# Optimization experiments

Hardware: AMD Instinct MI355X
Metric: run time of the kernel (lower is better)

Reference implementation:

```python
import jax, jax.numpy as jnp
import numpy as np

B, S, HID = 1, 2048, 2048
H = 16
D_NOPE, D_ROPE, D_V = 128, 64, 128
Q_HEAD = D_NOPE + D_ROPE  # 192
QL, KVL = 1536, 512
EPS = 1e-6
SCALE = Q_HEAD ** -0.5


def rms_norm(x, w, eps=EPS):
    return x * jax.lax.rsqrt(jnp.mean(x * x, axis=-1, keepdims=True) + eps) * w


def rotate_half(x):
    h = x.shape[-1] // 2
    return jnp.concatenate([-x[..., h:], x[..., :h]], axis=-1)


def apply_rope(x, cos, sin):
    # DeepSeek de-interleave: view(..., d//2, 2).transpose(-1,-2).reshape == [even, odd]
    x = jnp.concatenate([x[..., 0::2], x[..., 1::2]], axis=-1)
    return x * cos + rotate_half(x) * sin


def setup_inputs() -> dict:
    key = jax.random.key(0)
    ks = jax.random.split(key, 8)
    x = jax.random.normal(ks[0], (B, S, HID), dtype=jnp.float32)
    # causal additive mask
    causal = jnp.tril(jnp.ones((S, S), dtype=bool))
    mask = jnp.where(causal, 0.0, -1e9).astype(jnp.float32)[None, None]
    position_ids = jnp.broadcast_to(jnp.arange(S, dtype=jnp.int32), (B, S))
    # RoPE caches, theta=10000
    inv_freq = 1.0 / (10000.0 ** (np.arange(0, D_ROPE, 2, dtype=np.float32) / D_ROPE))
    freqs = np.outer(np.arange(S, dtype=np.float32), inv_freq)
    emb = np.concatenate([freqs, freqs], axis=-1)
    cos = jnp.asarray(np.cos(emb), dtype=jnp.float32)
    sin = jnp.asarray(np.sin(emb), dtype=jnp.float32)
    w = lambda k, shp: (jax.random.normal(k, shp, dtype=jnp.float32) * 0.02)
    return {
        "x": x, "mask": mask, "position_ids": position_ids, "cos": cos, "sin": sin,
        "q_a_w": w(ks[1], (HID, QL)),
        "q_a_ln": jnp.ones((QL,), jnp.float32),
        "q_b_w": w(ks[2], (QL, H * Q_HEAD)),
        "kv_a_w": w(ks[3], (HID, KVL + D_ROPE)),
        "kv_a_ln": jnp.ones((KVL,), jnp.float32),
        "kv_b_w": w(ks[4], (KVL, H * (D_NOPE + D_V))),
        "o_w": w(ks[5], (H * D_V, HID)),
    }


def reference(x, mask, position_ids, cos, sin, q_a_w, q_a_ln, q_b_w, kv_a_w, kv_a_ln, kv_b_w, o_w):
    b, s, _ = x.shape
    # low-rank Q projection
    q = rms_norm(x @ q_a_w, q_a_ln) @ q_b_w            # [B,S,H*192]
    q = q.reshape(b, s, H, Q_HEAD).transpose(0, 2, 1, 3)  # [B,H,S,192]
    q_nope, q_pe = q[..., :D_NOPE], q[..., D_NOPE:]
    # compressed KV + decoupled rope key (MQA, shared across heads)
    ckv = x @ kv_a_w                                   # [B,S,512+64]
    c_norm = rms_norm(ckv[..., :KVL], kv_a_ln)         # [B,S,512]
    k_pe = ckv[..., KVL:][:, None]                     # [B,1,S,64]
    kv = (c_norm @ kv_b_w).reshape(b, s, H, D_NOPE + D_V).transpose(0, 2, 1, 3)
    k_nope, value = kv[..., :D_NOPE], kv[..., D_NOPE:]  # [B,H,S,128] each
    # rope
    cos_p = cos[position_ids][:, None]                 # [B,1,S,64]
    sin_p = sin[position_ids][:, None]
    q_pe = apply_rope(q_pe, cos_p, sin_p)
    k_pe = apply_rope(k_pe, cos_p, sin_p)
    query = jnp.concatenate([q_nope, q_pe], axis=-1)   # [B,H,S,192]
    key = jnp.concatenate([k_nope, jnp.broadcast_to(k_pe, (b, H, s, D_ROPE))], axis=-1)
    scores = jnp.einsum("bhsd,bhtd->bhst", query, key) * SCALE + mask
    attn = jax.nn.softmax(scores, axis=-1)
    out = jnp.einsum("bhst,bhtd->bhsd", attn, value)   # [B,H,S,128]
    out = out.transpose(0, 2, 1, 3).reshape(b, s, H * D_V) @ o_w
    kv_cache = jnp.concatenate([c_norm, k_pe[:, 0]], axis=-1)  # [B,S,576] latent cache
    return out, kv_cache
```

## Files before the change

kernel.cpp:

```cpp
#include <hip/hip_runtime.h>

typedef unsigned short u16;
typedef __bf16 bf16x8 __attribute__((ext_vector_type(8)));
typedef short s16x4 __attribute__((ext_vector_type(4)));
typedef short s16x8 __attribute__((ext_vector_type(8)));
typedef float f32x4 __attribute__((ext_vector_type(4)));

#define S_LEN 2048
#define NHEAD 16
#define QHEAD 192
#define EPS 1e-6f
#define ATTN_SCALE 0.07216878364870323f
#define QSCALE_LOG2E 0.10412011228586118f

__device__ __forceinline__ u16 f2bf(float f) {
    unsigned u = __builtin_bit_cast(unsigned, f);
    u = (u + 0x7FFFu + ((u >> 16) & 1u)) >> 16;
    return (u16)u;
}
__device__ __forceinline__ float bf2f(u16 h) {
    unsigned u = ((unsigned)h) << 16;
    return __builtin_bit_cast(float, u);
}

__device__ __forceinline__ void gl_lds16(const u16* g, u16* l) {
    __builtin_amdgcn_global_load_lds(
        (const __attribute__((address_space(1))) unsigned int*)g,
        (__attribute__((address_space(3))) unsigned int*)l,
        16, 0, 0);
}

#if defined(__has_builtin) && __has_builtin(__builtin_amdgcn_mfma_f32_16x16x16bf16_1k)
__device__ __forceinline__ f32x4 mfma16(s16x4 a, s16x4 b, f32x4 c) {
    return __builtin_amdgcn_mfma_f32_16x16x16bf16_1k(a, b, c, 0, 0, 0);
}
#else
__device__ __forceinline__ f32x4 mfma16(s16x4 a, s16x4 b, f32x4 c) {
    asm volatile("v_mfma_f32_16x16x16_bf16 %0, %1, %2, %0"
                 : "+v"(c) : "v"(a), "v"(b));
    return c;
}
#endif

template <int CF32>
__device__ __forceinline__ void gemm_core(
    u16* __restrict__ smem,
    const u16* __restrict__ A, const u16* __restrict__ B, void* __restrict__ Cv,
    int K, int lda, int ldb, int ldc, int tm, int tn)
{
    const int tid = threadIdx.x;
    const int w = tid >> 6, lane = tid & 63;
    const int q = lane >> 4, r = lane & 15;

    const int lr = lane & 15;
    const int lc = (lane >> 4) * 8;
    const long ld = (w < 4) ? (long)lda : (long)ldb;
    const u16* g0 = ((w < 4)
        ? A + (long)(tm * 128 + w * 32 + lr) * lda
        : B + (long)(tn * 128 + (w - 4) * 32 + lr) * ldb) + lc;
    const u16* g1 = g0 + 16 * ld;
    const int s0 = w * 1024;
    const int s1 = s0 + 512;

    f32x4 acc[4][2] = {};
    const int wm = w >> 2;
    const int wn = w & 3;
    const int n = K >> 5;

    gl_lds16(g0, smem + s0);
    gl_lds16(g1, smem + s1);
    gl_lds16(g0 + 32, smem + 8192 + s0);
    gl_lds16(g1 + 32, smem + 8192 + s1);
    asm volatile("s_waitcnt vmcnt(2)" ::: "memory");
    __builtin_amdgcn_sched_barrier(0);
    __builtin_amdgcn_s_barrier();
    __builtin_amdgcn_sched_barrier(0);

    int bc = 0;
    for (int t = 0; t < n; ++t) {
        u16* const cur = smem + bc * 8192;
        if (t + 2 < n) {
            int bn = bc + 2; if (bn >= 3) bn -= 3;
            u16* const nxt = smem + bn * 8192;
            const long k2 = (long)(t + 2) << 5;
            gl_lds16(g0 + k2, nxt + s0);
            gl_lds16(g1 + k2, nxt + s1);
        }
        bf16x8 af[4], bv[2];
        #pragma unroll
        for (int mt = 0; mt < 4; ++mt)
            af[mt] = *(const bf16x8*)&cur[(wm * 4 + mt) * 512 + lane * 8];
        #pragma unroll
        for (int nt = 0; nt < 2; ++nt)
            bv[nt] = *(const bf16x8*)&cur[4096 + (wn * 2 + nt) * 512 + lane * 8];
        #pragma unroll
        for (int mt = 0; mt < 4; ++mt)
            #pragma unroll
            for (int nt = 0; nt < 2; ++nt)
                acc[mt][nt] = __builtin_amdgcn_mfma_f32_16x16x32_bf16(
                    af[mt], bv[nt], acc[mt][nt], 0, 0, 0);
        if (t + 1 < n) {
            if (t + 2 < n) asm volatile("s_waitcnt vmcnt(2)" ::: "memory");
            else           asm volatile("s_waitcnt vmcnt(0)" ::: "memory");
            __builtin_amdgcn_sched_barrier(0);
            __builtin_amdgcn_s_barrier();
            __builtin_amdgcn_sched_barrier(0);
        }
        if (++bc == 3) bc = 0;
    }

    const int row0 = tm * 128 + wm * 64 + q * 4;
    const int col0 = tn * 128 + wn * 32 + r;
    if (CF32) {
        float* C = (float*)Cv;
        #pragma unroll
        for (int mt = 0; mt < 4; ++mt)
            #pragma unroll
            for (int i = 0; i < 4; ++i) {
                long rb = (long)(row0 + mt * 16 + i) * ldc + col0;
                #pragma unroll
                for (int nt = 0; nt < 2; ++nt)
                    C[rb + nt * 16] = acc[mt][nt][i];
            }
    } else {
        u16* C = (u16*)Cv;
        #pragma unroll
        for (int mt = 0; mt < 4; ++mt)
            #pragma unroll
            for (int i = 0; i < 4; ++i) {
                long rb = (long)(row0 + mt * 16 + i) * ldc + col0;
                #pragma unroll
                for (int nt = 0; nt < 2; ++nt)
                    C[rb + nt * 16] = f2bf(acc[mt][nt][i]);
            }
    }
}

template <int CF32>
__global__ __launch_bounds__(512, 4)
void gemm_bt(const u16* __restrict__ A, const u16* __restrict__ B,
             void* __restrict__ Cv, int K, int lda, int ldb, int ldc)
{
    __shared__ __align__(16) u16 smem[3 * 8192];
    gemm_core<CF32>(smem, A, B, Cv, K, lda, ldb, ldc, blockIdx.y, blockIdx.x);
}

__global__ __launch_bounds__(512, 4)
void gemm_bt_dual(const u16* __restrict__ A0, const u16* __restrict__ B0,
                  void* __restrict__ C0, int K0, int lda0, int ldb0, int ldc0, int nx0,
                  const u16* __restrict__ A1, const u16* __restrict__ B1,
                  void* __restrict__ C1, int K1, int lda1, int ldb1, int ldc1, int nx1)
{
    __shared__ __align__(16) u16 smem[3 * 8192];
    if (blockIdx.z == 0) {
        if ((int)blockIdx.x >= nx0) return;
        gemm_core<0>(smem, A0, B0, C0, K0, lda0, ldb0, ldc0, blockIdx.y, blockIdx.x);
    } else {
        if ((int)blockIdx.x >= nx1) return;
        gemm_core<0>(smem, A1, B1, C1, K1, lda1, ldb1, ldc1, blockIdx.y, blockIdx.x);
    }
}

template<int C0, int C1>
__device__ __forceinline__ void stage_tile(
    const u16* __restrict__ kvb, const u16* __restrict__ kpe,
    const u16* __restrict__ vt,
    u16* __restrict__ Kl, u16* __restrict__ Vl,
    int h, int t, int quad, int r)
{
    #pragma unroll
    for (int c = C0; c < C1; ++c) {
        if (c < 24) {
            const int mtk = c / 6, kc = c % 6;
            const int row = t * 64 + mtk * 16 + r;
            const u16* src = (kc < 4)
                ? kvb + (size_t)row * 4096 + h * 256 + kc * 32 + quad * 8
                : kpe + (size_t)row * 64 + (kc - 4) * 32 + quad * 8;
            gl_lds16(src, &Kl[c * 512]);
        } else {
            const int cv = c - 24, mtd = cv >> 1, sc = cv & 1;
            const u16* src = vt + ((size_t)h * 128 + mtd * 16 + r) * 2048
                             + t * 64 + sc * 32 + quad * 8;
            gl_lds16(src, &Vl[cv * 512]);
        }
    }
}

__device__ __forceinline__ void stage_dispatch(
    const u16* __restrict__ kvb, const u16* __restrict__ kpe,
    const u16* __restrict__ vt,
    u16* __restrict__ Kl, u16* __restrict__ Vl,
    int w, int h, int t, int quad, int r)
{
    if (w == 0)      stage_tile<0, 10>(kvb, kpe, vt, Kl, Vl, h, t, quad, r);
    else if (w == 1) stage_tile<10, 20>(kvb, kpe, vt, Kl, Vl, h, t, quad, r);
    else if (w == 2) stage_tile<20, 30>(kvb, kpe, vt, Kl, Vl, h, t, quad, r);
    else             stage_tile<30, 40>(kvb, kpe, vt, Kl, Vl, h, t, quad, r);
}

__device__ __forceinline__ void kv_tile_step(
    const u16* __restrict__ Kl, const u16* __restrict__ Vl,
    const bf16x8 (&Qf)[6], f32x4 (&Oacc)[8], float& lsum,
    int lane, int quad, int r, int kglob0, int qg, bool maskT)
{
    f32x4 Sacc[4];
    #pragma unroll
    for (int mtk = 0; mtk < 4; ++mtk)
        Sacc[mtk] = (f32x4){0.f, 0.f, 0.f, 0.f};
    #pragma unroll
    for (int kc = 0; kc < 6; ++kc)
        #pragma unroll
        for (int mtk = 0; mtk < 4; ++mtk) {
            bf16x8 Ak = *(const bf16x8*)&Kl[(mtk * 6 + kc) * 512 + lane * 8];
            Sacc[mtk] = __builtin_amdgcn_mfma_f32_16x16x32_bf16(
                Ak, Qf[kc], Sacc[mtk], 0, 0, 0);
        }
    #pragma unroll
    for (int sc = 0; sc < 2; ++sc) {
        s16x4 Pf[2];
        #pragma unroll
        for (int half = 0; half < 2; ++half) {
            const int kb = sc * 2 + half;
            const int kb0 = kglob0 + kb * 16 + quad * 4;
            #pragma unroll
            for (int i = 0; i < 4; ++i) {
                float pv = exp2f(Sacc[kb][i]);
                if (maskT && (kb0 + i > qg)) pv = 0.f;
                lsum += pv;
                Pf[half][i] = (short)f2bf(pv);
            }
        }
        #pragma unroll
        for (int mtd = 0; mtd < 8; ++mtd) {
            s16x8 Av8 = *(const s16x8*)&Vl[(mtd * 2 + sc) * 512 + quad * 128 + r * 8];
            s16x4 lo = __builtin_shufflevector(Av8, Av8, 0, 1, 2, 3);
            s16x4 hi = __builtin_shufflevector(Av8, Av8, 4, 5, 6, 7);
            Oacc[mtd] = mfma16(lo, Pf[0], Oacc[mtd]);
            Oacc[mtd] = mfma16(hi, Pf[1], Oacc[mtd]);
        }
    }
}

__global__ __launch_bounds__(256, 2)
void flash_attn(const u16* __restrict__ query, const u16* __restrict__ kvb,
                const u16* __restrict__ kpe, const u16* __restrict__ vt,
                u16* __restrict__ ao)
{
    const int tid = threadIdx.x;
    const int w = tid >> 6, lane = tid & 63;
    const int quad = lane >> 4, r = lane & 15;

    const int bid = (int)blockIdx.x;
    const int i = bid & 255;
    const int t_ = i >> 4;
    const int h = i & 15;
    const int j = (bid < 256) ? (31 - t_) : t_;

    const int q0 = j * 64;
    const int ntk = j + 1;

    __shared__ __align__(16) u16 smem[40960];

    const int qg = q0 + w * 16 + r;

    bf16x8 Qf[6];
    #pragma unroll
    for (int kc = 0; kc < 6; ++kc)
        Qf[kc] = *(const bf16x8*)(query
            + ((size_t)h * S_LEN + q0 + w * 16 + r) * QHEAD
            + kc * 32 + quad * 8);

    f32x4 Oacc[8];
    #pragma unroll
    for (int mtd = 0; mtd < 8; ++mtd)
        Oacc[mtd] = (f32x4){0.f, 0.f, 0.f, 0.f};
    float lsum = 0.f;

    stage_dispatch(kvb, kpe, vt, smem, smem + 12288, w, h, 0, quad, r);
    __syncthreads();

    for (int t = 0; t < ntk; ++t) {
        u16* const curb = smem + (t & 1) * 20480;
        u16* const nxtb = smem + ((t + 1) & 1) * 20480;
        if (t + 1 < ntk)
            stage_dispatch(kvb, kpe, vt, nxtb, nxtb + 12288, w, h, t + 1, quad, r);
        kv_tile_step(curb, curb + 12288, Qf, Oacc, lsum,
                     lane, quad, r, t * 64, qg, t == ntk - 1);
        __syncthreads();
    }

    float l = lsum;
    l += __shfl_xor(l, 16, 64);
    l += __shfl_xor(l, 32, 64);
    const float inv = 1.0f / l;
    const int qrow = q0 + w * 16 + r;
    #pragma unroll
    for (int mtd = 0; mtd < 8; ++mtd) {
        ushort4 o;
        o.x = f2bf(Oacc[mtd][0] * inv);
        o.y = f2bf(Oacc[mtd][1] * inv);
        o.z = f2bf(Oacc[mtd][2] * inv);
        o.w = f2bf(Oacc[mtd][3] * inv);
        *(ushort4*)(ao + (size_t)qrow * 2048 + h * 128 + mtd * 16 + quad * 4) = o;
    }
}

__global__ __launch_bounds__(256)
void cvt_f32_bf16(const float4* __restrict__ in, ushort4* __restrict__ out, int n4)
{
    int i = blockIdx.x * 256 + threadIdx.x;
    if (i < n4) {
        float4 v = in[i];
        ushort4 o;
        o.x = f2bf(v.x); o.y = f2bf(v.y); o.z = f2bf(v.z); o.w = f2bf(v.w);
        out[i] = o;
    }
}

__global__ __launch_bounds__(256)
void wtrans_k(const float* __restrict__ in, u16* __restrict__ out, int K, int N)
{
    __shared__ float tile[32][33];
    int k0 = blockIdx.x * 32, n0 = blockIdx.y * 32;
    int tx = threadIdx.x, ty = threadIdx.y;
    #pragma unroll
    for (int j = 0; j < 32; j += 8) {
        int n = n0 + tx;
        tile[ty + j][tx] = (n < N) ? in[(long)(k0 + ty + j) * N + n] : 0.0f;
    }
    __syncthreads();
    #pragma unroll
    for (int j = 0; j < 32; j += 8)
        out[(long)(n0 + ty + j) * K + k0 + tx] = f2bf(tile[tx][ty + j]);
}

__global__ __launch_bounds__(256)
void rmsnorm_k(u16* __restrict__ X, const float* __restrict__ w, int D, int ld)
{
    u16* row = X + (long)blockIdx.x * ld;
    const int tid = threadIdx.x;
    __shared__ float red[4];
    float sum = 0.f;
    for (int d = tid; d < D; d += 256) { float v = bf2f(row[d]); sum += v * v; }
    #pragma unroll
    for (int o = 32; o; o >>= 1) sum += __shfl_xor(sum, o, 64);
    if ((tid & 63) == 0) red[tid >> 6] = sum;
    __syncthreads();
    sum = red[0] + red[1] + red[2] + red[3];
    float scale = rsqrtf(sum / (float)D + EPS);
    for (int d = tid; d < D; d += 256)
        row[d] = f2bf(bf2f(row[d]) * scale * w[d]);
}

__global__ __launch_bounds__(256)
void kvcache_k(const u16* __restrict__ qkv, const float* __restrict__ ln,
               const int* __restrict__ pos_ids, const float* __restrict__ cosb,
               const float* __restrict__ sinb, float* __restrict__ kvout,
               u16* __restrict__ cnb, u16* __restrict__ kpe)
{
    const int s = blockIdx.x, tid = threadIdx.x;
    const u16* row = qkv + (long)s * 2176 + 1536;
    __shared__ float red[4];
    float sum = 0.f;
    for (int d = tid; d < 512; d += 256) { float v = bf2f(row[d]); sum += v * v; }
    #pragma unroll
    for (int o = 32; o; o >>= 1) sum += __shfl_xor(sum, o, 64);
    if ((tid & 63) == 0) red[tid >> 6] = sum;
    __syncthreads();
    sum = red[0] + red[1] + red[2] + red[3];
    float scale = rsqrtf(sum / 512.f + EPS);
    for (int d = tid; d < 512; d += 256) {
        float v = bf2f(row[d]) * scale * ln[d];
        kvout[(long)s * 576 + d] = v;
        cnb[(long)s * 512 + d] = f2bf(v);
    }
    if (tid < 32) {
        int p = pos_ids[s];
        float x0 = bf2f(row[512 + 2 * tid]);
        float x1 = bf2f(row[512 + 2 * tid + 1]);
        float c1 = cosb[p * 64 + tid], s1 = sinb[p * 64 + tid];
        float c2 = cosb[p * 64 + 32 + tid], s2 = sinb[p * 64 + 32 + tid];
        float lo = x0 * c1 - x1 * s1;
        float hi = x1 * c2 + x0 * s2;
        kvout[(long)s * 576 + 512 + tid] = lo;
        kvout[(long)s * 576 + 544 + tid] = hi;
        kpe[(long)s * 64 + tid] = f2bf(lo);
        kpe[(long)s * 64 + 32 + tid] = f2bf(hi);
    }
}

__global__ __launch_bounds__(256)
void qrope_k(const u16* __restrict__ qb, const int* __restrict__ pos_ids,
             const float* __restrict__ cosb, const float* __restrict__ sinb,
             u16* __restrict__ query)
{
    const int s = blockIdx.x, tid = threadIdx.x;
    const u16* row = qb + (long)s * 3072;
    {
        int h = tid >> 4, c = tid & 15;
        const u16* src = &row[h * QHEAD + c * 8];
        u16* dst = &query[((long)(h * S_LEN + s)) * QHEAD + c * 8];
        ushort4 a = *(const ushort4*)src;
        ushort4 b = *(const ushort4*)(src + 4);
        ushort4 oa, ob;
        oa.x = f2bf(bf2f(a.x) * QSCALE_LOG2E); oa.y = f2bf(bf2f(a.y) * QSCALE_LOG2E);
        oa.z = f2bf(bf2f(a.z) * QSCALE_LOG2E); oa.w = f2bf(bf2f(a.w) * QSCALE_LOG2E);
        ob.x = f2bf(bf2f(b.x) * QSCALE_LOG2E); ob.y = f2bf(bf2f(b.y) * QSCALE_LOG2E);
        ob.z = f2bf(bf2f(b.z) * QSCALE_LOG2E); ob.w = f2bf(bf2f(b.w) * QSCALE_LOG2E);
        *(ushort4*)dst = oa;
        *(ushort4*)(dst + 4) = ob;
    }
    int p = pos_ids[s];
    for (int idx = tid; idx < 512; idx += 256) {
        int h = idx >> 5, i = idx & 31;
        float x0 = bf2f(row[h * QHEAD + 128 + 2 * i]);
        float x1 = bf2f(row[h * QHEAD + 128 + 2 * i + 1]);
        float c1 = cosb[p * 64 + i], s1 = sinb[p * 64 + i];
        float c2 = cosb[p * 64 + 32 + i], s2 = sinb[p * 64 + 32 + i];
        u16* qr = query + ((long)(h * S_LEN + s)) * QHEAD;
        qr[128 + i] = f2bf((x0 * c1 - x1 * s1) * QSCALE_LOG2E);
        qr[160 + i] = f2bf((x1 * c2 + x0 * s2) * QSCALE_LOG2E);
    }
}

__global__ __launch_bounds__(256)
void vtrans_k(const u16* __restrict__ kv, u16* __restrict__ vt)
{
    __shared__ u16 tile[32][33];
    int s0 = blockIdx.x * 32, d0 = blockIdx.y * 32, h = blockIdx.z;
    int tx = threadIdx.x, ty = threadIdx.y;
    #pragma unroll
    for (int j = 0; j < 32; j += 8)
        tile[ty + j][tx] = kv[(long)(s0 + ty + j) * 4096 + h * 256 + 128 + d0 + tx];
    __syncthreads();
    const int txp = ((tx >> 2) & 3) * 8 + (tx >> 4) * 4 + (tx & 3);
    #pragma unroll
    for (int j = 0; j < 32; j += 8)
        vt[(long)(h * 128 + d0 + ty + j) * S_LEN + s0 + txp] = tile[tx][ty + j];
}

extern "C" void kernel_launch(void* const* d_in, const int* in_sizes, int n_in,
                              void* d_out, int out_size, void* d_ws, size_t ws_size,
                              hipStream_t stream)
{
    const float* x      = (const float*)d_in[0];
    const int*   posid  = (const int*)d_in[2];
    const float* cosb   = (const float*)d_in[3];
    const float* sinb   = (const float*)d_in[4];
    const float* q_a_w  = (const float*)d_in[5];
    const float* q_a_ln = (const float*)d_in[6];
    const float* q_b_w  = (const float*)d_in[7];
    const float* kv_a_w = (const float*)d_in[8];
    const float* kv_a_ln= (const float*)d_in[9];
    const float* kv_b_w = (const float*)d_in[10];
    const float* o_w    = (const float*)d_in[11];

    float* out    = (float*)d_out;
    float* kv_out = out + (size_t)2048 * 2048;

    char* ws = (char*)d_ws;
    size_t off = 0;
    auto alloc = [&](size_t bytes) { char* p = ws + off; off += (bytes + 255) & ~(size_t)255; return p; };
    u16* xb    = (u16*)alloc(2048ULL * 2048 * 2);
    u16* W1    = (u16*)alloc(2176ULL * 2048 * 2);
    u16* qbwt  = (u16*)alloc(3072ULL * 1536 * 2);
    u16* kvbwt = (u16*)alloc(4096ULL * 512 * 2);
    u16* owt   = (u16*)alloc(2048ULL * 2048 * 2);
    u16* qkv_a = (u16*)alloc(2048ULL * 2176 * 2);
    u16* qbuf  = (u16*)alloc(2048ULL * 3072 * 2);
    u16* query = (u16*)alloc(16ULL * 2048 * 192 * 2);
    u16* cnb   = (u16*)alloc(2048ULL * 512 * 2);
    u16* kpe   = (u16*)alloc(2048ULL * 64 * 2);
    u16* kvbuf = (u16*)alloc(2048ULL * 4096 * 2);
    u16* vt    = (u16*)alloc(16ULL * 128 * 2048 * 2);
    u16* ao    = (u16*)alloc(2048ULL * 2048 * 2);
    (void)ws_size; (void)in_sizes; (void)n_in; (void)out_size;

    dim3 blk(256);
    dim3 gblk(512);
    dim3 tblk(32, 8);

    cvt_f32_bf16<<<dim3(4096), blk, 0, stream>>>((const float4*)x, (ushort4*)xb, 2048 * 2048 / 4);
    wtrans_k<<<dim3(64, 48),  tblk, 0, stream>>>(q_a_w,  W1,                    2048, 1536);
    wtrans_k<<<dim3(64, 20),  tblk, 0, stream>>>(kv_a_w, W1 + 1536ULL * 2048,   2048, 576);
    wtrans_k<<<dim3(48, 96),  tblk, 0, stream>>>(q_b_w,  qbwt,  1536, 3072);
    wtrans_k<<<dim3(16, 128), tblk, 0, stream>>>(kv_b_w, kvbwt, 512,  4096);
    wtrans_k<<<dim3(64, 64),  tblk, 0, stream>>>(o_w,    owt,   2048, 2048);

    gemm_bt<0><<<dim3(17, 16), gblk, 0, stream>>>(xb, W1, qkv_a, 2048, 2048, 2048, 2176);
    rmsnorm_k<<<dim3(2048), blk, 0, stream>>>(qkv_a, q_a_ln, 1536, 2176);
    kvcache_k<<<dim3(2048), blk, 0, stream>>>(qkv_a, kv_a_ln, posid, cosb, sinb, kv_out, cnb, kpe);

    gemm_bt_dual<<<dim3(32, 16, 2), gblk, 0, stream>>>(
        qkv_a, qbwt, qbuf, 1536, 2176, 1536, 3072, 24,
        cnb, kvbwt, kvbuf, 512, 512, 512, 4096, 32);
    qrope_k<<<dim3(2048), blk, 0, stream>>>(qbuf, posid, cosb, sinb, query);
    vtrans_k<<<dim3(64, 4, 16), tblk, 0, stream>>>(kvbuf, vt);

    flash_attn<<<dim3(512), dim3(256), 0, stream>>>(query, kvbuf, kpe, vt, ao);

    gemm_bt<1><<<dim3(16, 16), gblk, 0, stream>>>(ao, owt, out, 2048, 2048, 2048, 2048);
}
```

Measured before the change: 397.4 us.

## Fuse prep/norm/post kernels and double per-wave tile work in GEMM and attention

Merges the input cast and five weight transposes into one launch, the two RMSNorm kernels into one, and the q-rope and V-transpose kernels into one, cutting the launch count. The GEMM drops from 8 to 4 waves per block, with each wave computing a 64x64 sub-tile instead of 64x32 and issuing both A and B loads. Flash attention drops from 4 to 2 waves, each handling 32 query rows so every K fragment read from LDS feeds two MFMAs. The larger per-wave tiles raise register pressure and lower occupancy, which could reduce latency hiding.

```diff
diff --git a/kernel.cpp b/kernel.cpp
--- a/kernel.cpp
+++ b/kernel.cpp
@@ -54,24 +54,27 @@
 
     const int lr = lane & 15;
     const int lc = (lane >> 4) * 8;
-    const long ld = (w < 4) ? (long)lda : (long)ldb;
-    const u16* g0 = ((w < 4)
-        ? A + (long)(tm * 128 + w * 32 + lr) * lda
-        : B + (long)(tn * 128 + (w - 4) * 32 + lr) * ldb) + lc;
-    const u16* g1 = g0 + 16 * ld;
-    const int s0 = w * 1024;
-    const int s1 = s0 + 512;
-
-    f32x4 acc[4][2] = {};
-    const int wm = w >> 2;
-    const int wn = w & 3;
+    const u16* ga0 = A + (long)(tm * 128 + w * 32 + lr) * lda + lc;
+    const u16* ga1 = ga0 + 16 * (long)lda;
+    const u16* gb0 = B + (long)(tn * 128 + w * 32 + lr) * ldb + lc;
+    const u16* gb1 = gb0 + 16 * (long)ldb;
+    const int sa0 = w * 1024, sa1 = sa0 + 512;
+    const int sb0 = 4096 + w * 1024, sb1 = sb0 + 512;
+
+    f32x4 acc[4][4] = {};
+    const int wm = w >> 1;
+    const int wn = w & 1;
     const int n = K >> 5;
 
-    gl_lds16(g0, smem + s0);
-    gl_lds16(g1, smem + s1);
-    gl_lds16(g0 + 32, smem + 8192 + s0);
-    gl_lds16(g1 + 32, smem + 8192 + s1);
-    asm volatile("s_waitcnt vmcnt(2)" ::: "memory");
+    gl_lds16(ga0, smem + sa0);
+    gl_lds16(ga1, smem + sa1);
+    gl_lds16(gb0, smem + sb0);
+    gl_lds16(gb1, smem + sb1);
+    gl_lds16(ga0 + 32, smem + 8192 + sa0);
+    gl_lds16(ga1 + 32, smem + 8192 + sa1);
+    gl_lds16(gb0 + 32, smem + 8192 + sb0);
+    gl_lds16(gb1 + 32, smem + 8192 + sb1);
+    asm volatile("s_waitcnt vmcnt(4)" ::: "memory");
     __builtin_amdgcn_sched_barrier(0);
     __builtin_amdgcn_s_barrier();
     __builtin_amdgcn_sched_barrier(0);
@@ -83,24 +86,26 @@
             int bn = bc + 2; if (bn >= 3) bn -= 3;
             u16* const nxt = smem + bn * 8192;
             const long k2 = (long)(t + 2) << 5;
-            gl_lds16(g0 + k2, nxt + s0);
-            gl_lds16(g1 + k2, nxt + s1);
-        }
-        bf16x8 af[4], bv[2];
+            gl_lds16(ga0 + k2, nxt + sa0);
+            gl_lds16(ga1 + k2, nxt + sa1);
+            gl_lds16(gb0 + k2, nxt + sb0);
+            gl_lds16(gb1 + k2, nxt + sb1);
+        }
+        bf16x8 af[4], bv[4];
         #pragma unroll
         for (int mt = 0; mt < 4; ++mt)
             af[mt] = *(const bf16x8*)&cur[(wm * 4 + mt) * 512 + lane * 8];
         #pragma unroll
-        for (int nt = 0; nt < 2; ++nt)
-            bv[nt] = *(const bf16x8*)&cur[4096 + (wn * 2 + nt) * 512 + lane * 8];
+        for (int nt = 0; nt < 4; ++nt)
+            bv[nt] = *(const bf16x8*)&cur[4096 + (wn * 4 + nt) * 512 + lane * 8];
         #pragma unroll
         for (int mt = 0; mt < 4; ++mt)
             #pragma unroll
-            for (int nt = 0; nt < 2; ++nt)
+            for (int nt = 0; nt < 4; ++nt)
                 acc[mt][nt] = __builtin_amdgcn_mfma_f32_16x16x32_bf16(
                     af[mt], bv[nt], acc[mt][nt], 0, 0, 0);
         if (t + 1 < n) {
-            if (t + 2 < n) asm volatile("s_waitcnt vmcnt(2)" ::: "memory");
+            if (t + 2 < n) asm volatile("s_waitcnt vmcnt(4)" ::: "memory");
             else           asm volatile("s_waitcnt vmcnt(0)" ::: "memory");
             __builtin_amdgcn_sched_barrier(0);
             __builtin_amdgcn_s_barrier();
@@ -110,7 +115,7 @@
     }
 
     const int row0 = tm * 128 + wm * 64 + q * 4;
-    const int col0 = tn * 128 + wn * 32 + r;
+    const int col0 = tn * 128 + wn * 64 + r;
     if (CF32) {
         float* C = (float*)Cv;
         #pragma unroll
@@ -119,7 +124,7 @@
             for (int i = 0; i < 4; ++i) {
                 long rb = (long)(row0 + mt * 16 + i) * ldc + col0;
                 #pragma unroll
-                for (int nt = 0; nt < 2; ++nt)
+                for (int nt = 0; nt < 4; ++nt)
                     C[rb + nt * 16] = acc[mt][nt][i];
             }
     } else {
@@ -130,14 +135,14 @@
             for (int i = 0; i < 4; ++i) {
                 long rb = (long)(row0 + mt * 16 + i) * ldc + col0;
                 #pragma unroll
-                for (int nt = 0; nt < 2; ++nt)
+                for (int nt = 0; nt < 4; ++nt)
                     C[rb + nt * 16] = f2bf(acc[mt][nt][i]);
             }
     }
 }
 
 template <int CF32>
-__global__ __launch_bounds__(512, 4)
+__global__ __launch_bounds__(256, 2)
 void gemm_bt(const u16* __restrict__ A, const u16* __restrict__ B,
              void* __restrict__ Cv, int K, int lda, int ldb, int ldc)
 {
@@ -145,7 +150,7 @@
     gemm_core<CF32>(smem, A, B, Cv, K, lda, ldb, ldc, blockIdx.y, blockIdx.x);
 }
 
-__global__ __launch_bounds__(512, 4)
+__global__ __launch_bounds__(256, 2)
 void gemm_bt_dual(const u16* __restrict__ A0, const u16* __restrict__ B0,
                   void* __restrict__ C0, int K0, int lda0, int ldb0, int ldc0, int nx0,
                   const u16* __restrict__ A1, const u16* __restrict__ B1,
@@ -192,42 +197,48 @@
     u16* __restrict__ Kl, u16* __restrict__ Vl,
     int w, int h, int t, int quad, int r)
 {
-    if (w == 0)      stage_tile<0, 10>(kvb, kpe, vt, Kl, Vl, h, t, quad, r);
-    else if (w == 1) stage_tile<10, 20>(kvb, kpe, vt, Kl, Vl, h, t, quad, r);
-    else if (w == 2) stage_tile<20, 30>(kvb, kpe, vt, Kl, Vl, h, t, quad, r);
-    else             stage_tile<30, 40>(kvb, kpe, vt, Kl, Vl, h, t, quad, r);
+    if (w == 0) stage_tile<0, 20>(kvb, kpe, vt, Kl, Vl, h, t, quad, r);
+    else        stage_tile<20, 40>(kvb, kpe, vt, Kl, Vl, h, t, quad, r);
 }
 
 __device__ __forceinline__ void kv_tile_step(
     const u16* __restrict__ Kl, const u16* __restrict__ Vl,
-    const bf16x8 (&Qf)[6], f32x4 (&Oacc)[8], float& lsum,
-    int lane, int quad, int r, int kglob0, int qg, bool maskT)
-{
-    f32x4 Sacc[4];
-    #pragma unroll
-    for (int mtk = 0; mtk < 4; ++mtk)
-        Sacc[mtk] = (f32x4){0.f, 0.f, 0.f, 0.f};
+    const bf16x8 (&Qf)[2][6], f32x4 (&Oacc)[8][2], float (&lsum)[2],
+    int lane, int quad, int r, int kglob0, int qg0, int qg1, bool maskT)
+{
+    f32x4 Sacc[4][2];
+    #pragma unroll
+    for (int mtk = 0; mtk < 4; ++mtk) {
+        Sacc[mtk][0] = (f32x4){0.f, 0.f, 0.f, 0.f};
+        Sacc[mtk][1] = (f32x4){0.f, 0.f, 0.f, 0.f};
+    }
     #pragma unroll
     for (int kc = 0; kc < 6; ++kc)
         #pragma unroll
         for (int mtk = 0; mtk < 4; ++mtk) {
             bf16x8 Ak = *(const bf16x8*)&Kl[(mtk * 6 + kc) * 512 + lane * 8];
-            Sacc[mtk] = __builtin_amdgcn_mfma_f32_16x16x32_bf16(
-                Ak, Qf[kc], Sacc[mtk], 0, 0, 0);
+            Sacc[mtk][0] = __builtin_amdgcn_mfma_f32_16x16x32_bf16(
+                Ak, Qf[0][kc], Sacc[mtk][0], 0, 0, 0);
+            Sacc[mtk][1] = __builtin_amdgcn_mfma_f32_16x16x32_bf16(
+                Ak, Qf[1][kc], Sacc[mtk][1], 0, 0, 0);
         }
     #pragma unroll
     for (int sc = 0; sc < 2; ++sc) {
-        s16x4 Pf[2];
-        #pragma unroll
-        for (int half = 0; half < 2; ++half) {
-            const int kb = sc * 2 + half;
-            const int kb0 = kglob0 + kb * 16 + quad * 4;
+        s16x4 Pf[2][2];
+        #pragma unroll
+        for (int nn = 0; nn < 2; ++nn) {
+            const int qg = nn ? qg1 : qg0;
             #pragma unroll
-            for (int i = 0; i < 4; ++i) {
-                float pv = exp2f(Sacc[kb][i]);
-                if (maskT && (kb0 + i > qg)) pv = 0.f;
-                lsum += pv;
-                Pf[half][i] = (short)f2bf(pv);
+            for (int half = 0; half < 2; ++half) {
+                const int kb = sc * 2 + half;
+                const int kb0 = kglob0 + kb * 16 + quad * 4;
+                #pragma unroll
+                for (int i = 0; i < 4; ++i) {
+                    float pv = exp2f(Sacc[kb][nn][i]);
+                    if (maskT && (kb0 + i > qg)) pv = 0.f;
+                    lsum[nn] += pv;
+                    Pf[nn][half][i] = (short)f2bf(pv);
+                }
             }
         }
         #pragma unroll
@@ -235,13 +246,15 @@
             s16x8 Av8 = *(const s16x8*)&Vl[(mtd * 2 + sc) * 512 + quad * 128 + r * 8];
             s16x4 lo = __builtin_shufflevector(Av8, Av8, 0, 1, 2, 3);
             s16x4 hi = __builtin_shufflevector(Av8, Av8, 4, 5, 6, 7);
-            Oacc[mtd] = mfma16(lo, Pf[0], Oacc[mtd]);
-            Oacc[mtd] = mfma16(hi, Pf[1], Oacc[mtd]);
-        }
-    }
-}
-
-__global__ __launch_bounds__(256, 2)
+            Oacc[mtd][0] = mfma16(lo, Pf[0][0], Oacc[mtd][0]);
+            Oacc[mtd][0] = mfma16(hi, Pf[0][1], Oacc[mtd][0]);
+            Oacc[mtd][1] = mfma16(lo, Pf[1][0], Oacc[mtd][1]);
+            Oacc[mtd][1] = mfma16(hi, Pf[1][1], Oacc[mtd][1]);
+        }
+    }
+}
+
+__global__ __launch_bounds__(128, 1)
 void flash_attn(const u16* __restrict__ query, const u16* __restrict__ kvb,
                 const u16* __restrict__ kpe, const u16* __restrict__ vt,
                 u16* __restrict__ ao)
@@ -261,20 +274,25 @@
 
     __shared__ __align__(16) u16 smem[40960];
 
-    const int qg = q0 + w * 16 + r;
-
-    bf16x8 Qf[6];
-    #pragma unroll
-    for (int kc = 0; kc < 6; ++kc)
-        Qf[kc] = *(const bf16x8*)(query
-            + ((size_t)h * S_LEN + q0 + w * 16 + r) * QHEAD
-            + kc * 32 + quad * 8);
-
-    f32x4 Oacc[8];
-    #pragma unroll
-    for (int mtd = 0; mtd < 8; ++mtd)
-        Oacc[mtd] = (f32x4){0.f, 0.f, 0.f, 0.f};
-    float lsum = 0.f;
+    const int qg0 = q0 + w * 32 + r;
+    const int qg1 = qg0 + 16;
+
+    bf16x8 Qf[2][6];
+    #pragma unroll
+    for (int nn = 0; nn < 2; ++nn)
+        #pragma unroll
+        for (int kc = 0; kc < 6; ++kc)
+            Qf[nn][kc] = *(const bf16x8*)(query
+                + ((size_t)h * S_LEN + q0 + w * 32 + nn * 16 + r) * QHEAD
+                + kc * 32 + quad * 8);
+
+    f32x4 Oacc[8][2];
+    #pragma unroll
+    for (int mtd = 0; mtd < 8; ++mtd) {
+        Oacc[mtd][0] = (f32x4){0.f, 0.f, 0.f, 0.f};
+        Oacc[mtd][1] = (f32x4){0.f, 0.f, 0.f, 0.f};
+    }
+    float lsum[2] = {0.f, 0.f};
 
     stage_dispatch(kvb, kpe, vt, smem, smem + 12288, w, h, 0, quad, r);
     __syncthreads();
@@ -285,99 +303,110 @@
         if (t + 1 < ntk)
             stage_dispatch(kvb, kpe, vt, nxtb, nxtb + 12288, w, h, t + 1, quad, r);
         kv_tile_step(curb, curb + 12288, Qf, Oacc, lsum,
-                     lane, quad, r, t * 64, qg, t == ntk - 1);
+                     lane, quad, r, t * 64, qg0, qg1, t == ntk - 1);
         __syncthreads();
     }
 
-    float l = lsum;
-    l += __shfl_xor(l, 16, 64);
-    l += __shfl_xor(l, 32, 64);
-    const float inv = 1.0f / l;
-    const int qrow = q0 + w * 16 + r;
-    #pragma unroll
-    for (int mtd = 0; mtd < 8; ++mtd) {
-        ushort4 o;
-        o.x = f2bf(Oacc[mtd][0] * inv);
-        o.y = f2bf(Oacc[mtd][1] * inv);
-        o.z = f2bf(Oacc[mtd][2] * inv);
-        o.w = f2bf(Oacc[mtd][3] * inv);
-        *(ushort4*)(ao + (size_t)qrow * 2048 + h * 128 + mtd * 16 + quad * 4) = o;
-    }
+    #pragma unroll
+    for (int nn = 0; nn < 2; ++nn) {
+        float l = lsum[nn];
+        l += __shfl_xor(l, 16, 64);
+        l += __shfl_xor(l, 32, 64);
+        const float inv = 1.0f / l;
+        const int qrow = q0 + w * 32 + nn * 16 + r;
+        #pragma unroll
+        for (int mtd = 0; mtd < 8; ++mtd) {
+            ushort4 o;
+            o.x = f2bf(Oacc[mtd][nn][0] * inv);
+            o.y = f2bf(Oacc[mtd][nn][1] * inv);
+            o.z = f2bf(Oacc[mtd][nn][2] * inv);
+            o.w = f2bf(Oacc[mtd][nn][3] * inv);
+            *(ushort4*)(ao + (size_t)qrow * 2048 + h * 128 + mtd * 16 + quad * 4) = o;
+        }
+    }
+}
+
+__device__ __forceinline__ void wtrans_body(
+    float (*tile)[33], const float* __restrict__ in, u16* __restrict__ out,
+    int K, int N, int bx, int by, int tid)
+{
+    const int tx = tid & 31, ty = tid >> 5;
+    const int k0 = bx * 32, n0 = by * 32;
+    #pragma unroll
+    for (int jj = 0; jj < 32; jj += 8) {
+        int nn = n0 + tx;
+        tile[ty + jj][tx] = (nn < N) ? in[(long)(k0 + ty + jj) * N + nn] : 0.0f;
+    }
+    __syncthreads();
+    #pragma unroll
+    for (int jj = 0; jj < 32; jj += 8)
+        out[(long)(n0 + ty + jj) * K + k0 + tx] = f2bf(tile[tx][ty + jj]);
 }
 
 __global__ __launch_bounds__(256)
-void cvt_f32_bf16(const float4* __restrict__ in, ushort4* __restrict__ out, int n4)
-{
-    int i = blockIdx.x * 256 + threadIdx.x;
-    if (i < n4) {
-        float4 v = in[i];
+void prep_k(const float4* __restrict__ x4, ushort4* __restrict__ xb4,
+            const float* __restrict__ q_a_w, const float* __restrict__ kv_a_w,
+            const float* __restrict__ q_b_w, const float* __restrict__ kv_b_w,
+            const float* __restrict__ o_w,
+            u16* __restrict__ W1, u16* __restrict__ qbwt,
+            u16* __restrict__ kvbwt, u16* __restrict__ owt)
+{
+    __shared__ float tile[32][33];
+    const int tid = threadIdx.x;
+    int b = (int)blockIdx.x;
+    if (b < 4096) {
+        int i = b * 256 + tid;
+        float4 v = x4[i];
         ushort4 o;
         o.x = f2bf(v.x); o.y = f2bf(v.y); o.z = f2bf(v.z); o.w = f2bf(v.w);
-        out[i] = o;
-    }
+        xb4[i] = o;
+        return;
+    }
+    b -= 4096;
+    if (b < 3072)       wtrans_body(tile, q_a_w,  W1,                  2048, 1536, b % 64, b / 64, tid);
+    else if ((b -= 3072) < 1280) wtrans_body(tile, kv_a_w, W1 + 1536ULL * 2048, 2048, 576,  b % 64, b / 64, tid);
+    else if ((b -= 1280) < 4608) wtrans_body(tile, q_b_w,  qbwt,       1536, 3072, b % 48, b / 48, tid);
+    else if ((b -= 4608) < 2048) wtrans_body(tile, kv_b_w, kvbwt,      512,  4096, b % 16, b / 16, tid);
+    else { b -= 2048;            wtrans_body(tile, o_w,    owt,        2048, 2048, b % 64, b / 64, tid); }
 }
 
 __global__ __launch_bounds__(256)
-void wtrans_k(const float* __restrict__ in, u16* __restrict__ out, int K, int N)
-{
-    __shared__ float tile[32][33];
-    int k0 = blockIdx.x * 32, n0 = blockIdx.y * 32;
-    int tx = threadIdx.x, ty = threadIdx.y;
-    #pragma unroll
-    for (int j = 0; j < 32; j += 8) {
-        int n = n0 + tx;
-        tile[ty + j][tx] = (n < N) ? in[(long)(k0 + ty + j) * N + n] : 0.0f;
-    }
-    __syncthreads();
-    #pragma unroll
-    for (int j = 0; j < 32; j += 8)
-        out[(long)(n0 + ty + j) * K + k0 + tx] = f2bf(tile[tx][ty + j]);
-}
-
-__global__ __launch_bounds__(256)
-void rmsnorm_k(u16* __restrict__ X, const float* __restrict__ w, int D, int ld)
-{
-    u16* row = X + (long)blockIdx.x * ld;
-    const int tid = threadIdx.x;
-    __shared__ float red[4];
+void norm_k(u16* __restrict__ qkv, const float* __restrict__ q_ln,
+            const float* __restrict__ kv_ln, const int* __restrict__ pos_ids,
+            const float* __restrict__ cosb, const float* __restrict__ sinb,
+            float* __restrict__ kvout, u16* __restrict__ cnb,
+            u16* __restrict__ kpe)
+{
+    const int s = blockIdx.x, tid = threadIdx.x;
+    u16* row = qkv + (long)s * 2176;
+    u16* row2 = row + 1536;
+    __shared__ float red[8];
     float sum = 0.f;
-    for (int d = tid; d < D; d += 256) { float v = bf2f(row[d]); sum += v * v; }
+    for (int d = tid; d < 1536; d += 256) { float v = bf2f(row[d]); sum += v * v; }
     #pragma unroll
     for (int o = 32; o; o >>= 1) sum += __shfl_xor(sum, o, 64);
     if ((tid & 63) == 0) red[tid >> 6] = sum;
+    float sum2 = 0.f;
+    for (int d = tid; d < 512; d += 256) { float v = bf2f(row2[d]); sum2 += v * v; }
+    #pragma unroll
+    for (int o = 32; o; o >>= 1) sum2 += __shfl_xor(sum2, o, 64);
+    if ((tid & 63) == 0) red[4 + (tid >> 6)] = sum2;
     __syncthreads();
-    sum = red[0] + red[1] + red[2] + red[3];
-    float scale = rsqrtf(sum / (float)D + EPS);
-    for (int d = tid; d < D; d += 256)
-        row[d] = f2bf(bf2f(row[d]) * scale * w[d]);
-}
-
-__global__ __launch_bounds__(256)
-void kvcache_k(const u16* __restrict__ qkv, const float* __restrict__ ln,
-               const int* __restrict__ pos_ids, const float* __restrict__ cosb,
-               const float* __restrict__ sinb, float* __restrict__ kvout,
-               u16* __restrict__ cnb, u16* __restrict__ kpe)
-{
-    const int s = blockIdx.x, tid = threadIdx.x;
-    const u16* row = qkv + (long)s * 2176 + 1536;
-    __shared__ float red[4];
-    float sum = 0.f;
-    for (int d = tid; d < 512; d += 256) { float v = bf2f(row[d]); sum += v * v; }
-    #pragma unroll
-    for (int o = 32; o; o >>= 1) sum += __shfl_xor(sum, o, 64);
-    if ((tid & 63) == 0) red[tid >> 6] = sum;
-    __syncthreads();
-    sum = red[0] + red[1] + red[2] + red[3];
-    float scale = rsqrtf(sum / 512.f + EPS);
+    sum  = red[0] + red[1] + red[2] + red[3];
+    sum2 = red[4] + red[5] + red[6] + red[7];
+    const float sc1 = rsqrtf(sum / 1536.f + EPS);
+    const float sc2 = rsqrtf(sum2 / 512.f + EPS);
+    for (int d = tid; d < 1536; d += 256)
+        row[d] = f2bf(bf2f(row[d]) * sc1 * q_ln[d]);
     for (int d = tid; d < 512; d += 256) {
-        float v = bf2f(row[d]) * scale * ln[d];
+        float v = bf2f(row2[d]) * sc2 * kv_ln[d];
         kvout[(long)s * 576 + d] = v;
         cnb[(long)s * 512 + d] = f2bf(v);
     }
     if (tid < 32) {
         int p = pos_ids[s];
-        float x0 = bf2f(row[512 + 2 * tid]);
-        float x1 = bf2f(row[512 + 2 * tid + 1]);
+        float x0 = bf2f(row2[512 + 2 * tid]);
+        float x1 = bf2f(row2[512 + 2 * tid + 1]);
         float c1 = cosb[p * 64 + tid], s1 = sinb[p * 64 + tid];
         float c2 = cosb[p * 64 + 32 + tid], s2 = sinb[p * 64 + 32 + tid];
         float lo = x0 * c1 - x1 * s1;
@@ -390,53 +419,55 @@
 }
 
 __global__ __launch_bounds__(256)
-void qrope_k(const u16* __restrict__ qb, const int* __restrict__ pos_ids,
-             const float* __restrict__ cosb, const float* __restrict__ sinb,
-             u16* __restrict__ query)
-{
-    const int s = blockIdx.x, tid = threadIdx.x;
-    const u16* row = qb + (long)s * 3072;
-    {
-        int h = tid >> 4, c = tid & 15;
-        const u16* src = &row[h * QHEAD + c * 8];
-        u16* dst = &query[((long)(h * S_LEN + s)) * QHEAD + c * 8];
-        ushort4 a = *(const ushort4*)src;
-        ushort4 b = *(const ushort4*)(src + 4);
-        ushort4 oa, ob;
-        oa.x = f2bf(bf2f(a.x) * QSCALE_LOG2E); oa.y = f2bf(bf2f(a.y) * QSCALE_LOG2E);
-        oa.z = f2bf(bf2f(a.z) * QSCALE_LOG2E); oa.w = f2bf(bf2f(a.w) * QSCALE_LOG2E);
-        ob.x = f2bf(bf2f(b.x) * QSCALE_LOG2E); ob.y = f2bf(bf2f(b.y) * QSCALE_LOG2E);
-        ob.z = f2bf(bf2f(b.z) * QSCALE_LOG2E); ob.w = f2bf(bf2f(b.w) * QSCALE_LOG2E);
-        *(ushort4*)dst = oa;
-        *(ushort4*)(dst + 4) = ob;
-    }
-    int p = pos_ids[s];
-    for (int idx = tid; idx < 512; idx += 256) {
-        int h = idx >> 5, i = idx & 31;
-        float x0 = bf2f(row[h * QHEAD + 128 + 2 * i]);
-        float x1 = bf2f(row[h * QHEAD + 128 + 2 * i + 1]);
-        float c1 = cosb[p * 64 + i], s1 = sinb[p * 64 + i];
-        float c2 = cosb[p * 64 + 32 + i], s2 = sinb[p * 64 + 32 + i];
-        u16* qr = query + ((long)(h * S_LEN + s)) * QHEAD;
-        qr[128 + i] = f2bf((x0 * c1 - x1 * s1) * QSCALE_LOG2E);
-        qr[160 + i] = f2bf((x1 * c2 + x0 * s2) * QSCALE_LOG2E);
-    }
-}
-
-__global__ __launch_bounds__(256)
-void vtrans_k(const u16* __restrict__ kv, u16* __restrict__ vt)
+void post_k(const u16* __restrict__ qb, const int* __restrict__ pos_ids,
+            const float* __restrict__ cosb, const float* __restrict__ sinb,
+            u16* __restrict__ query, const u16* __restrict__ kv,
+            u16* __restrict__ vt)
 {
     __shared__ u16 tile[32][33];
-    int s0 = blockIdx.x * 32, d0 = blockIdx.y * 32, h = blockIdx.z;
-    int tx = threadIdx.x, ty = threadIdx.y;
-    #pragma unroll
-    for (int j = 0; j < 32; j += 8)
-        tile[ty + j][tx] = kv[(long)(s0 + ty + j) * 4096 + h * 256 + 128 + d0 + tx];
-    __syncthreads();
-    const int txp = ((tx >> 2) & 3) * 8 + (tx >> 4) * 4 + (tx & 3);
-    #pragma unroll
-    for (int j = 0; j < 32; j += 8)
-        vt[(long)(h * 128 + d0 + ty + j) * S_LEN + s0 + txp] = tile[tx][ty + j];
+    const int tid = threadIdx.x;
+    int b = (int)blockIdx.x;
+    if (b < 2048) {
+        const int s = b;
+        const u16* row = qb + (long)s * 3072;
+        {
+            int h = tid >> 4, c = tid & 15;
+            const u16* src = &row[h * QHEAD + c * 8];
+            u16* dst = &query[((long)(h * S_LEN + s)) * QHEAD + c * 8];
+            ushort4 a = *(const ushort4*)src;
+            ushort4 bb = *(const ushort4*)(src + 4);
+            ushort4 oa, ob;
+            oa.x = f2bf(bf2f(a.x) * QSCALE_LOG2E); oa.y = f2bf(bf2f(a.y) * QSCALE_LOG2E);
+            oa.z = f2bf(bf2f(a.z) * QSCALE_LOG2E); oa.w = f2bf(bf2f(a.w) * QSCALE_LOG2E);
+            ob.x = f2bf(bf2f(bb.x) * QSCALE_LOG2E); ob.y = f2bf(bf2f(bb.y) * QSCALE_LOG2E);
+            ob.z = f2bf(bf2f(bb.z) * QSCALE_LOG2E); ob.w = f2bf(bf2f(bb.w) * QSCALE_LOG2E);
+            *(ushort4*)dst = oa;
+            *(ushort4*)(dst + 4) = ob;
+        }
+        int p = pos_ids[s];
+        for (int idx = tid; idx < 512; idx += 256) {
+            int h = idx >> 5, i = idx & 31;
+            float x0 = bf2f(row[h * QHEAD + 128 + 2 * i]);
+            float x1 = bf2f(row[h * QHEAD + 128 + 2 * i + 1]);
+            float c1 = cosb[p * 64 + i], s1 = sinb[p * 64 + i];
+            float c2 = cosb[p * 64 + 32 + i], s2 = sinb[p * 64 + 32 + i];
+            u16* qr = query + ((long)(h * S_LEN + s)) * QHEAD;
+            qr[128 + i] = f2bf((x0 * c1 - x1 * s1) * QSCALE_LOG2E);
+            qr[160 + i] = f2bf((x1 * c2 + x0 * s2) * QSCALE_LOG2E);
+        }
+    } else {
+        b -= 2048;
+        const int s0 = (b & 63) * 32, d0 = ((b >> 6) & 3) * 32, h = b >> 8;
+        const int tx = tid & 31, ty = tid >> 5;
+        #pragma unroll
+        for (int jj = 0; jj < 32; jj += 8)
+            tile[ty + jj][tx] = kv[(long)(s0 + ty + jj) * 4096 + h * 256 + 128 + d0 + tx];
+        __syncthreads();
+        const int txp = ((tx >> 2) & 3) * 8 + (tx >> 4) * 4 + (tx & 3);
+        #pragma unroll
+        for (int jj = 0; jj < 32; jj += 8)
+            vt[(long)(h * 128 + d0 + ty + jj) * S_LEN + s0 + txp] = tile[tx][ty + jj];
+    }
 }
 
 extern "C" void kernel_launch(void* const* d_in, const int* in_sizes, int n_in,
@@ -477,27 +508,23 @@
     (void)ws_size; (void)in_sizes; (void)n_in; (void)out_size;
 
     dim3 blk(256);
-    dim3 gblk(512);
-    dim3 tblk(32, 8);
-
-    cvt_f32_bf16<<<dim3(4096), blk, 0, stream>>>((const float4*)x, (ushort4*)xb, 2048 * 2048 / 4);
-    wtrans_k<<<dim3(64, 48),  tblk, 0, stream>>>(q_a_w,  W1,                    2048, 1536);
-    wtrans_k<<<dim3(64, 20),  tblk, 0, stream>>>(kv_a_w, W1 + 1536ULL * 2048,   2048, 576);
-    wtrans_k<<<dim3(48, 96),  tblk, 0, stream>>>(q_b_w,  qbwt,  1536, 3072);
-    wtrans_k<<<dim3(16, 128), tblk, 0, stream>>>(kv_b_w, kvbwt, 512,  4096);
-    wtrans_k<<<dim3(64, 64),  tblk, 0, stream>>>(o_w,    owt,   2048, 2048);
-
-    gemm_bt<0><<<dim3(17, 16), gblk, 0, stream>>>(xb, W1, qkv_a, 2048, 2048, 2048, 2176);
-    rmsnorm_k<<<dim3(2048), blk, 0, stream>>>(qkv_a, q_a_ln, 1536, 2176);
-    kvcache_k<<<dim3(2048), blk, 0, stream>>>(qkv_a, kv_a_ln, posid, cosb, sinb, kv_out, cnb, kpe);
-
-    gemm_bt_dual<<<dim3(32, 16, 2), gblk, 0, stream>>>(
+
+    prep_k<<<dim3(19200), blk, 0, stream>>>(
+        (const float4*)x, (ushort4*)xb, q_a_w, kv_a_w, q_b_w, kv_b_w, o_w,
+        W1, qbwt, kvbwt, owt);
+
+    gemm_bt<0><<<dim3(17, 16), blk, 0, stream>>>(xb, W1, qkv_a, 2048, 2048, 2048, 2176);
+
+    norm_k<<<dim3(2048), blk, 0, stream>>>(qkv_a, q_a_ln, kv_a_ln, posid,
+                                           cosb, sinb, kv_out, cnb, kpe);
+
+    gemm_bt_dual<<<dim3(32, 16, 2), blk, 0, stream>>>(
         qkv_a, qbwt, qbuf, 1536, 2176, 1536, 3072, 24,
         cnb, kvbwt, kvbuf, 512, 512, 512, 4096, 32);
-    qrope_k<<<dim3(2048), blk, 0, stream>>>(qbuf, posid, cosb, sinb, query);
-    vtrans_k<<<dim3(64, 4, 16), tblk, 0, stream>>>(kvbuf, vt);
-
-    flash_attn<<<dim3(512), dim3(256), 0, stream>>>(query, kvbuf, kpe, vt, ao);
-
-    gemm_bt<1><<<dim3(16, 16), gblk, 0, stream>>>(ao, owt, out, 2048, 2048, 2048, 2048);
-}
+
+    post_k<<<dim3(6144), blk, 0, stream>>>(qbuf, posid, cosb, sinb, query, kvbuf, vt);
+
+    flash_attn<<<dim3(512), dim3(128), 0, stream>>>(query, kvbuf, kpe, vt, ao);
+
+    gemm_bt<1><<<dim3(16, 16), blk, 0, stream>>>(ao, owt, out, 2048, 2048, 2048, 2048);
+}
```

New measurement: 427.7 us. 7.6% more time.
